# Kernel optimization log

Hardware: AMD Instinct MI355X
Metric: run time of the kernel (lower is better)

Reference implementation:

```python
import jax, jax.numpy as jnp
import numpy as np

B, N, DIN, DOUT, S, ITERS = 32, 2048, 512, 512, 2, 3
HID = max(DOUT, 128)  # mlp hidden = max(dim_out, hidden_dim)
EPS = 1e-8
LN_EPS = 1e-5  # torch LayerNorm default
SCALE = DOUT ** -0.5


def layernorm(x, g, b):
    m = jnp.mean(x, axis=-1, keepdims=True)
    v = jnp.mean(jnp.square(x - m), axis=-1, keepdims=True)
    return (x - m) * jax.lax.rsqrt(v + LN_EPS) * g + b


def setup_inputs() -> dict:
    key = jax.random.key(0)
    ks = jax.random.split(key, 16)
    w = lambda k, shp: jax.random.normal(k, shp, dtype=jnp.float32) * 0.02
    return {
        "inputs": jax.random.normal(ks[0], (B, N, DIN), dtype=jnp.float32),
        "shared_init_slots": jax.random.normal(ks[1], (B, S, DOUT), dtype=jnp.float32),
        "Wq": w(ks[2], (DOUT, DOUT)), "bq": jnp.zeros((DOUT,), jnp.float32),
        "Wk": w(ks[3], (DIN, DOUT)), "bk": jnp.zeros((DOUT,), jnp.float32),
        "Wv": w(ks[4], (DIN, DOUT)), "bv": jnp.zeros((DOUT,), jnp.float32),
        "ln_in_g": jnp.ones((DIN,), jnp.float32), "ln_in_b": jnp.zeros((DIN,), jnp.float32),
        "ln_s_g": jnp.ones((DOUT,), jnp.float32), "ln_s_b": jnp.zeros((DOUT,), jnp.float32),
        "ln_f_g": jnp.ones((DOUT,), jnp.float32), "ln_f_b": jnp.zeros((DOUT,), jnp.float32),
        "gru_wih": w(ks[5], (3 * DOUT, DOUT)), "gru_whh": w(ks[6], (3 * DOUT, DOUT)),
        "gru_bih": jnp.zeros((3 * DOUT,), jnp.float32), "gru_bhh": jnp.zeros((3 * DOUT,), jnp.float32),
        "W1": w(ks[7], (DOUT, HID)), "b1": jnp.zeros((HID,), jnp.float32),
        "W2": w(ks[8], (HID, DOUT)), "b2": jnp.zeros((DOUT,), jnp.float32),
    }


def reference(inputs, shared_init_slots, Wq, bq, Wk, bk, Wv, bv,
              ln_in_g, ln_in_b, ln_s_g, ln_s_b, ln_f_g, ln_f_b,
              gru_wih, gru_whh, gru_bih, gru_bhh, W1, b1, W2, b2):
    x = layernorm(inputs, ln_in_g, ln_in_b)          # [B,N,DIN]
    k = x @ Wk + bk                                   # [B,N,DOUT]
    v = x @ Wv + bv                                   # [B,N,DOUT]
    slots = shared_init_slots                         # [B,S,DOUT]
    for _ in range(ITERS):
        slots_prev = slots
        s = layernorm(slots, ln_s_g, ln_s_b)
        q = s @ Wq + bq                               # [B,S,DOUT]
        dots = jnp.einsum('bid,bjd->bij', q, k) * SCALE   # [B,S,N]
        attn_pre = jax.nn.softmax(dots, axis=1)       # softmax over SLOT dim (custom)
        attn = attn_pre / (jnp.sum(attn_pre, axis=-1, keepdims=True) + EPS)
        updates = jnp.einsum('bjd,bij->bid', v, attn)  # [B,S,DOUT]
        # GRUCell: h' = (1-z)*n + z*h, gate order r,z,n (torch convention)
        u = updates.reshape(-1, DOUT)
        h = slots_prev.reshape(-1, DOUT)
        gx = u @ gru_wih.T + gru_bih                  # [B*S, 3*DOUT]
        gh = h @ gru_whh.T + gru_bhh
        xr, xz, xn = jnp.split(gx, 3, axis=-1)
        hr, hz, hn = jnp.split(gh, 3, axis=-1)
        r = jax.nn.sigmoid(xr + hr)
        z = jax.nn.sigmoid(xz + hz)
        n_gate = jnp.tanh(xn + r * hn)
        h_new = (1.0 - z) * n_gate + z * h
        # residual MLP
        hln = layernorm(h_new, ln_f_g, ln_f_b)
        h_new = h_new + (jax.nn.relu(hln @ W1 + b1) @ W2 + b2)
        slots = h_new.reshape(B, S, DOUT)
    return slots, q, k, attn
```

## Files before the change

kernel.cpp:

```cpp
#include <hip/hip_runtime.h>
#include <stdint.h>

typedef __bf16 bf16_t;
typedef bf16_t bf16x8 __attribute__((ext_vector_type(8)));
typedef float f32x4 __attribute__((ext_vector_type(4)));

typedef unsigned int u32;
typedef __attribute__((address_space(1))) const u32 gu32;
typedef __attribute__((address_space(3))) u32 lu32;

#define LN_EPS 1e-5f
#define EPS_ 1e-8f
#define SCALE_ 0.04419417382415922f

__device__ __forceinline__ float wave_red_sum(float v) {
#pragma unroll
  for (int off = 32; off > 0; off >>= 1) v += __shfl_xor(v, off, 64);
  return v;
}

__global__ __launch_bounds__(256) void transpose_prep(
    const float* __restrict__ Wk, const float* __restrict__ Wv,
    const float* __restrict__ wih, const float* __restrict__ whh,
    bf16_t* __restrict__ BT, float* __restrict__ wihT, float* __restrict__ whhT)
{
  int z = blockIdx.z;
  if (z < 2 && blockIdx.y >= 16) return;
  const float* src = (z == 0) ? Wk : (z == 1) ? Wv : (z == 2) ? wih : whh;
  __shared__ float tile[32][33];
  int tx = threadIdx.x & 31, ty = threadIdx.x >> 5;
  int row0 = blockIdx.y * 32, col0 = blockIdx.x * 32;
#pragma unroll
  for (int i = 0; i < 4; ++i)
    tile[ty + 8 * i][tx] = src[(size_t)(row0 + ty + 8 * i) * 512 + col0 + tx];
  __syncthreads();
  if (z < 2) {
#pragma unroll
    for (int i = 0; i < 4; ++i)
      BT[(size_t)(z * 512 + col0 + ty + 8 * i) * 512 + row0 + tx] =
          (bf16_t)tile[tx][ty + 8 * i];
  } else {
    float* dst = (z == 2) ? wihT : whhT;
#pragma unroll
    for (int i = 0; i < 4; ++i)
      dst[(size_t)(col0 + ty + 8 * i) * 1536 + row0 + tx] = tile[tx][ty + 8 * i];
  }
}

__global__ __launch_bounds__(256) void small_prep(
    const float* __restrict__ bk, const float* __restrict__ bv,
    const float* __restrict__ slots_init,
    float* __restrict__ biasc, float* __restrict__ slots)
{
  int idx = blockIdx.x * 256 + threadIdx.x;
  if (idx < 1024) {
    biasc[idx] = (idx < 512) ? bk[idx] : bv[idx - 512];
  } else {
    int i = idx - 1024;
    slots[i] = slots_init[i];
  }
}

__global__ __launch_bounds__(256) void ln_apply(
    const float* __restrict__ in, const float* __restrict__ lng,
    const float* __restrict__ lnb, bf16_t* __restrict__ xbf)
{
  int w = threadIdx.x >> 6, lane = threadIdx.x & 63;
  size_t row = (size_t)blockIdx.x * 4 + w;
  const float4* rp = (const float4*)(in + row * 512);
  float4 a = rp[lane * 2], c = rp[lane * 2 + 1];
  float s1 = a.x + a.y + a.z + a.w + c.x + c.y + c.z + c.w;
  float s2 = a.x * a.x + a.y * a.y + a.z * a.z + a.w * a.w +
             c.x * c.x + c.y * c.y + c.z * c.z + c.w * c.w;
  s1 = wave_red_sum(s1);
  s2 = wave_red_sum(s2);
  float mean = s1 * (1.f / 512.f);
  float var = s2 * (1.f / 512.f) - mean * mean;
  float rs = rsqrtf(var + LN_EPS);
  float4 g0 = *(const float4*)&lng[lane * 8];
  float4 g1 = *(const float4*)&lng[lane * 8 + 4];
  float4 b0 = *(const float4*)&lnb[lane * 8];
  float4 b1 = *(const float4*)&lnb[lane * 8 + 4];
  bf16x8 o;
  o[0] = (bf16_t)((a.x - mean) * rs * g0.x + b0.x);
  o[1] = (bf16_t)((a.y - mean) * rs * g0.y + b0.y);
  o[2] = (bf16_t)((a.z - mean) * rs * g0.z + b0.z);
  o[3] = (bf16_t)((a.w - mean) * rs * g0.w + b0.w);
  o[4] = (bf16_t)((c.x - mean) * rs * g1.x + b1.x);
  o[5] = (bf16_t)((c.y - mean) * rs * g1.y + b1.y);
  o[6] = (bf16_t)((c.z - mean) * rs * g1.z + b1.z);
  o[7] = (bf16_t)((c.w - mean) * rs * g1.w + b1.w);
  *(bf16x8*)&xbf[row * 512 + lane * 8] = o;
}

__global__ __launch_bounds__(256) void gemm_kv(
    const bf16_t* __restrict__ xbf, const bf16_t* __restrict__ BT,
    const float* __restrict__ biasc,
    float* __restrict__ out_k, bf16_t* __restrict__ vbf, bf16_t* kbf)
{
  __shared__ __align__(16) char smem[32768];
  bf16_t* As = (bf16_t*)smem;
  bf16_t* Bs = (bf16_t*)(smem + 16384);
  float (*Cs)[132] = (float(*)[132])smem;

  const int tid = threadIdx.x, lane = tid & 63, w = tid >> 6;
  const int quad = lane >> 4, l16 = lane & 15;
  const int l = blockIdx.x;
  const int x = l & 7, t = l >> 3;
  const int n0 = (t & 7) * 128;
  const int m0 = ((t >> 3) * 8 + x) * 128;
  const int mb = (w & 1) * 64, nb = (w >> 1) * 64;
  const int swz = l16 & 7;

  const bf16_t* a_base = xbf + (size_t)m0 * 512;
  const bf16_t* b_base = BT + (size_t)n0 * 512;

  f32x4 acc[4][4] = {};

  for (int kk = 0; kk < 512; kk += 64) {
#pragma unroll
    for (int r = 0; r < 4; ++r) {
      int tt = tid + r * 256;
      int rr = tt >> 3, pg = tt & 7;
      int lg = pg ^ (rr & 7);
      __builtin_amdgcn_global_load_lds((gu32*)(a_base + (size_t)rr * 512 + kk + lg * 8),
                                       (lu32*)&As[tt * 8], 16, 0, 0);
      __builtin_amdgcn_global_load_lds((gu32*)(b_base + (size_t)rr * 512 + kk + lg * 8),
                                       (lu32*)&Bs[tt * 8], 16, 0, 0);
    }
    __syncthreads();
#pragma unroll
    for (int ks = 0; ks < 2; ++ks) {
      bf16x8 af[4], bfr[4];
#pragma unroll
      for (int mt = 0; mt < 4; ++mt)
        af[mt] = *(const bf16x8*)&As[(mb + mt * 16 + l16) * 64 + (((quad + 4 * ks) ^ swz) * 8)];
#pragma unroll
      for (int nt = 0; nt < 4; ++nt)
        bfr[nt] = *(const bf16x8*)&Bs[(nb + nt * 16 + l16) * 64 + (((quad + 4 * ks) ^ swz) * 8)];
#pragma unroll
      for (int mt = 0; mt < 4; ++mt)
#pragma unroll
        for (int nt = 0; nt < 4; ++nt)
          acc[mt][nt] = __builtin_amdgcn_mfma_f32_16x16x32_bf16(af[mt], bfr[nt], acc[mt][nt], 0, 0, 0);
    }
    __syncthreads();
  }

  const int is_k = (n0 < 512);
  const int col4 = (tid * 4) & 127;
  const int row8 = tid >> 4;
  const int col8 = (tid * 8) & 127;
  for (int ci = 0; ci < 8; ++ci) {
    if ((ci < 4) == (mb == 0)) {
      int mt = ci & 3;
#pragma unroll
      for (int nt = 0; nt < 4; ++nt)
#pragma unroll
        for (int r = 0; r < 4; ++r)
          Cs[quad * 4 + r][nb + nt * 16 + l16] = acc[mt][nt][r];
    }
    __syncthreads();
    int rowbase = m0 + ci * 16;
    if (is_k) {
      f32x4 bias4 = *(const f32x4*)&biasc[n0 + col4];
#pragma unroll
      for (int p = 0; p < 2; ++p) {
        int f = p * 1024 + tid * 4;
        int row = f >> 7;
        f32x4 v = *(const f32x4*)&Cs[row][col4] + bias4;
        *(f32x4*)&out_k[(size_t)(rowbase + row) * 512 + n0 + col4] = v;
      }
      if (kbf) {
        f32x4 ba = *(const f32x4*)&biasc[n0 + col8];
        f32x4 bb = *(const f32x4*)&biasc[n0 + col8 + 4];
        f32x4 v0 = *(const f32x4*)&Cs[row8][col8] + ba;
        f32x4 v1 = *(const f32x4*)&Cs[row8][col8 + 4] + bb;
        bf16x8 o;
#pragma unroll
        for (int j = 0; j < 4; ++j) { o[j] = (bf16_t)v0[j]; o[4 + j] = (bf16_t)v1[j]; }
        *(bf16x8*)&kbf[(size_t)(rowbase + row8) * 512 + n0 + col8] = o;
      }
    } else {
      f32x4 ba = *(const f32x4*)&biasc[n0 + col8];
      f32x4 bb = *(const f32x4*)&biasc[n0 + col8 + 4];
      f32x4 v0 = *(const f32x4*)&Cs[row8][col8] + ba;
      f32x4 v1 = *(const f32x4*)&Cs[row8][col8 + 4] + bb;
      bf16x8 o;
#pragma unroll
      for (int j = 0; j < 4; ++j) { o[j] = (bf16_t)v0[j]; o[4 + j] = (bf16_t)v1[j]; }
      *(bf16x8*)&vbf[(size_t)(rowbase + row8) * 512 + (n0 - 512) + col8] = o;
    }
    __syncthreads();
  }
}

__global__ __launch_bounds__(256) void ln_q_kernel(
    const float* __restrict__ slots,
    const float* __restrict__ lnsg, const float* __restrict__ lnsb,
    const float* __restrict__ Wq, const float* __restrict__ bq,
    float* __restrict__ q_out)
{
  __shared__ float s[2][512];
  __shared__ float part[4][2][64];
  __shared__ float red1[4], red2[4];
  int tid = threadIdx.x, w = tid >> 6, lane = tid & 63;
  int b = blockIdx.x >> 3, cg = blockIdx.x & 7;

  int r = tid >> 7;
  int off = (tid * 4) & 511;
  float4 v = *(const float4*)&slots[b * 1024 + tid * 4];
  float s1 = v.x + v.y + v.z + v.w;
  float s2 = v.x * v.x + v.y * v.y + v.z * v.z + v.w * v.w;
  s1 = wave_red_sum(s1);
  s2 = wave_red_sum(s2);
  if (lane == 0) { red1[w] = s1; red2[w] = s2; }
  __syncthreads();
  float mean = (red1[r * 2] + red1[r * 2 + 1]) * (1.f / 512.f);
  float var = (red2[r * 2] + red2[r * 2 + 1]) * (1.f / 512.f) - mean * mean;
  float rstd = rsqrtf(var + LN_EPS);
  float4 g4 = *(const float4*)&lnsg[off];
  float4 b4 = *(const float4*)&lnsb[off];
  s[r][off + 0] = (v.x - mean) * rstd * g4.x + b4.x;
  s[r][off + 1] = (v.y - mean) * rstd * g4.y + b4.y;
  s[r][off + 2] = (v.z - mean) * rstd * g4.z + b4.z;
  s[r][off + 3] = (v.w - mean) * rstd * g4.w + b4.w;
  __syncthreads();

  int c = cg * 64 + lane;
  float a0 = 0.f, a1 = 0.f;
  for (int d = w * 128; d < w * 128 + 128; ++d) {
    float wv = Wq[d * 512 + c];
    a0 += s[0][d] * wv;
    a1 += s[1][d] * wv;
  }
  part[w][0][lane] = a0;
  part[w][1][lane] = a1;
  __syncthreads();
  if (tid < 128) {
    int rr = tid >> 6, ll = tid & 63;
    float sum = part[0][rr][ll] + part[1][rr][ll] + part[2][rr][ll] + part[3][rr][ll]
              + bq[cg * 64 + ll];
    q_out[(b * 2 + rr) * 512 + cg * 64 + ll] = sum;
  }
}

__global__ __launch_bounds__(256) void attend_fused(
    const float* __restrict__ kf, const bf16_t* __restrict__ vbf,
    const float* __restrict__ qf,
    float* __restrict__ upd_part, float* __restrict__ rs_part,
    float* __restrict__ attn_pre)
{
  __shared__ float qs[2][528];
  __shared__ float p_s[2][64];
  int tid = threadIdx.x, w = tid >> 6, lane = tid & 63;
  int b = blockIdx.x >> 5, chunk = blockIdx.x & 31;
  int j0 = chunk * 64;

  {
    int slot = tid >> 7, pos = (tid & 127) * 4;
    int dq = pos >> 7, dd = pos & 127;
    *(f32x4*)&qs[slot][dq * 132 + dd] = *(const f32x4*)&qf[b * 1024 + slot * 512 + pos];
  }
  __syncthreads();

  int jj = lane & 15;
  int dq = lane >> 4;
  const float* kp = kf + (size_t)(b * 2048 + j0 + w * 16 + jj) * 512 + dq * 128;
  const float* qb0 = &qs[0][dq * 132];
  const float* qb1 = &qs[1][dq * 132];
  float dot0 = 0.f, dot1 = 0.f;
#pragma unroll
  for (int h = 0; h < 4; ++h) {
    f32x4 kr[8];
#pragma unroll
    for (int i = 0; i < 8; ++i) kr[i] = *(const f32x4*)(kp + h * 32 + i * 4);
#pragma unroll
    for (int i = 0; i < 8; ++i) {
      f32x4 qa = *(const f32x4*)(qb0 + h * 32 + i * 4);
      f32x4 qc = *(const f32x4*)(qb1 + h * 32 + i * 4);
#pragma unroll
      for (int t = 0; t < 4; ++t) {
        dot0 += kr[i][t] * qa[t];
        dot1 += kr[i][t] * qc[t];
      }
    }
  }
  dot0 += __shfl_xor(dot0, 16, 64);
  dot0 += __shfl_xor(dot0, 32, 64);
  dot1 += __shfl_xor(dot1, 16, 64);
  dot1 += __shfl_xor(dot1, 32, 64);
  float d0f = dot0 * SCALE_, d1f = dot1 * SCALE_;
  float mx = fmaxf(d0f, d1f);
  float e0 = __expf(d0f - mx), e1 = __expf(d1f - mx);
  float inv = 1.f / (e0 + e1);
  float p0 = e0 * inv, p1 = e1 * inv;
  if (lane < 16) {
    int jj2 = w * 16 + lane;
    p_s[0][jj2] = p0;
    p_s[1][jj2] = p1;
    attn_pre[(b * 2 + 0) * 2048 + j0 + jj2] = p0;
    attn_pre[(b * 2 + 1) * 2048 + j0 + jj2] = p1;
  }
  __syncthreads();

  if (w == 0) {
    float a = p_s[0][lane];
    float c = p_s[1][lane];
    a = wave_red_sum(a);
    c = wave_red_sum(c);
    if (lane == 0) {
      rs_part[(b * 2 + 0) * 32 + chunk] = a;
      rs_part[(b * 2 + 1) * 32 + chunk] = c;
    }
  }

  float u0[8] = {}, u1[8] = {};
  const bf16_t* vp = vbf + (size_t)(b * 2048 + j0 + w * 16) * 512 + lane * 8;
  for (int t = 0; t < 16; ++t) {
    float p0b = p_s[0][w * 16 + t];
    float p1b = p_s[1][w * 16 + t];
    bf16x8 vv = *(const bf16x8*)(vp + (size_t)t * 512);
#pragma unroll
    for (int tt = 0; tt < 8; ++tt) {
      float vfl = (float)vv[tt];
      u0[tt] += p0b * vfl;
      u1[tt] += p1b * vfl;
    }
  }
  float* up0 = upd_part + ((size_t)(chunk * 4 + w) * 64 + b * 2 + 0) * 512 + lane * 8;
  f32x4 w0a = {u0[0], u0[1], u0[2], u0[3]}, w0b = {u0[4], u0[5], u0[6], u0[7]};
  f32x4 w1a = {u1[0], u1[1], u1[2], u1[3]}, w1b = {u1[4], u1[5], u1[6], u1[7]};
  *(f32x4*)(up0) = w0a;
  *(f32x4*)(up0 + 4) = w0b;
  *(f32x4*)(up0 + 512) = w1a;
  *(f32x4*)(up0 + 516) = w1b;
}

__global__ __launch_bounds__(256) void attend_bf16(
    const bf16_t* __restrict__ kbf, const bf16_t* __restrict__ vbf,
    const float* __restrict__ qf,
    float* __restrict__ upd_part, float* __restrict__ rs_part,
    float* __restrict__ attn_pre)
{
  __shared__ float qs[2][528];
  __shared__ float p_s[2][64];
  int tid = threadIdx.x, w = tid >> 6, lane = tid & 63;
  int b = blockIdx.x >> 5, chunk = blockIdx.x & 31;
  int j0 = chunk * 64;

  {
    int slot = tid >> 7, pos = (tid & 127) * 4;
    int dq = pos >> 7, dd = pos & 127;
    *(f32x4*)&qs[slot][dq * 132 + dd] = *(const f32x4*)&qf[b * 1024 + slot * 512 + pos];
  }
  __syncthreads();

  int jj = lane & 15;
  int dq = lane >> 4;
  const bf16_t* kp = kbf + (size_t)(b * 2048 + j0 + w * 16 + jj) * 512 + dq * 128;
  const float* qb0 = &qs[0][dq * 132];
  const float* qb1 = &qs[1][dq * 132];
  float dot0 = 0.f, dot1 = 0.f;
#pragma unroll
  for (int h = 0; h < 2; ++h) {
    bf16x8 kr[8];
#pragma unroll
    for (int i = 0; i < 8; ++i) kr[i] = *(const bf16x8*)(kp + h * 64 + i * 8);
#pragma unroll
    for (int i = 0; i < 8; ++i) {
      f32x4 qa0 = *(const f32x4*)(qb0 + h * 64 + i * 8);
      f32x4 qa1 = *(const f32x4*)(qb0 + h * 64 + i * 8 + 4);
      f32x4 qc0 = *(const f32x4*)(qb1 + h * 64 + i * 8);
      f32x4 qc1 = *(const f32x4*)(qb1 + h * 64 + i * 8 + 4);
#pragma unroll
      for (int t = 0; t < 4; ++t) {
        float klo = (float)kr[i][t], khi = (float)kr[i][t + 4];
        dot0 += klo * qa0[t] + khi * qa1[t];
        dot1 += klo * qc0[t] + khi * qc1[t];
      }
    }
  }
  dot0 += __shfl_xor(dot0, 16, 64);
  dot0 += __shfl_xor(dot0, 32, 64);
  dot1 += __shfl_xor(dot1, 16, 64);
  dot1 += __shfl_xor(dot1, 32, 64);
  float d0f = dot0 * SCALE_, d1f = dot1 * SCALE_;
  float mx = fmaxf(d0f, d1f);
  float e0 = __expf(d0f - mx), e1 = __expf(d1f - mx);
  float inv = 1.f / (e0 + e1);
  float p0 = e0 * inv, p1 = e1 * inv;
  if (lane < 16) {
    int jj2 = w * 16 + lane;
    p_s[0][jj2] = p0;
    p_s[1][jj2] = p1;
    attn_pre[(b * 2 + 0) * 2048 + j0 + jj2] = p0;
    attn_pre[(b * 2 + 1) * 2048 + j0 + jj2] = p1;
  }
  __syncthreads();

  if (w == 0) {
    float a = p_s[0][lane];
    float c = p_s[1][lane];
    a = wave_red_sum(a);
    c = wave_red_sum(c);
    if (lane == 0) {
      rs_part[(b * 2 + 0) * 32 + chunk] = a;
      rs_part[(b * 2 + 1) * 32 + chunk] = c;
    }
  }

  float u0[8] = {}, u1[8] = {};
  const bf16_t* vp = vbf + (size_t)(b * 2048 + j0 + w * 16) * 512 + lane * 8;
  for (int t = 0; t < 16; ++t) {
    float p0b = p_s[0][w * 16 + t];
    float p1b = p_s[1][w * 16 + t];
    bf16x8 vv = *(const bf16x8*)(vp + (size_t)t * 512);
#pragma unroll
    for (int tt = 0; tt < 8; ++tt) {
      float vfl = (float)vv[tt];
      u0[tt] += p0b * vfl;
      u1[tt] += p1b * vfl;
    }
  }
  float* up0 = upd_part + ((size_t)(chunk * 4 + w) * 64 + b * 2 + 0) * 512 + lane * 8;
  f32x4 w0a = {u0[0], u0[1], u0[2], u0[3]}, w0b = {u0[4], u0[5], u0[6], u0[7]};
  f32x4 w1a = {u1[0], u1[1], u1[2], u1[3]}, w1b = {u1[4], u1[5], u1[6], u1[7]};
  *(f32x4*)(up0) = w0a;
  *(f32x4*)(up0 + 4) = w0b;
  *(f32x4*)(up0 + 512) = w1a;
  *(f32x4*)(up0 + 516) = w1b;
}

__global__ __launch_bounds__(512) void reduce_upd(
    const float* __restrict__ upd_part, const float* __restrict__ rs_part,
    float* __restrict__ upd, float* __restrict__ rowsum)
{
  int r = blockIdx.x, tid = threadIdx.x;
  const float* p = upd_part + (size_t)r * 512 + tid;
  float acc = 0.f;
#pragma unroll 8
  for (int i = 0; i < 128; ++i) acc += p[(size_t)i * 32768];
  upd[r * 512 + tid] = acc;
  if (tid < 64) {
    float v = (tid < 32) ? rs_part[r * 32 + tid] : 0.f;
    v = wave_red_sum(v);
    if (tid == 0) rowsum[r] = v;
  }
}

__global__ __launch_bounds__(256) void gates_kernel(
    const float* __restrict__ slots, const float* __restrict__ upd,
    const float* __restrict__ rowsum,
    const float* __restrict__ wihT, const float* __restrict__ whhT,
    const float* __restrict__ bih, const float* __restrict__ bhh,
    float* __restrict__ gx, float* __restrict__ gh)
{
  __shared__ float in_s[2][512];
  __shared__ float part[4][2][256];
  int tid = threadIdx.x, w = tid >> 6, lane = tid & 63;
  int rg = blockIdx.x / 12, cc = blockIdx.x % 12;
  int is_gh = (cc >= 6);
  int ccl = is_gh ? cc - 6 : cc;
  {
    int rr = tid >> 7, pos = (tid & 127) * 4;
    int row = rg * 2 + rr;
    const float* src = (is_gh ? slots : upd) + row * 512;
    f32x4 v = *(const f32x4*)&src[pos];
    if (!is_gh) v *= 1.f / (rowsum[row] + EPS_);
    *(f32x4*)&in_s[rr][pos] = v;
  }
  __syncthreads();
  int c0 = ccl * 256 + lane * 4;
  const float* __restrict__ W = is_gh ? whhT : wihT;
  f32x4 acc0 = {0.f, 0.f, 0.f, 0.f}, acc1 = acc0;
  for (int d = w * 128; d < w * 128 + 128; ++d) {
    f32x4 w4 = *(const f32x4*)&W[d * 1536 + c0];
    acc0 += in_s[0][d] * w4;
    acc1 += in_s[1][d] * w4;
  }
  *(f32x4*)&part[w][0][lane * 4] = acc0;
  *(f32x4*)&part[w][1][lane * 4] = acc1;
  __syncthreads();
  if (tid < 128) {
    int r = tid >> 6, ll = tid & 63;
    int cf = ccl * 256 + ll * 4;
    f32x4 s = *(const f32x4*)&part[0][r][ll * 4];
    s += *(const f32x4*)&part[1][r][ll * 4];
    s += *(const f32x4*)&part[2][r][ll * 4];
    s += *(const f32x4*)&part[3][r][ll * 4];
    s += *(const f32x4*)&(is_gh ? bhh : bih)[cf];
    *(f32x4*)&(is_gh ? gh : gx)[(rg * 2 + r) * 1536 + cf] = s;
  }
}

__global__ __launch_bounds__(512) void gru_ln_kernel(
    const float* __restrict__ gx, const float* __restrict__ gh,
    const float* __restrict__ slots,
    const float* __restrict__ lnf_g, const float* __restrict__ lnf_b,
    float* __restrict__ hnew, float* __restrict__ hln)
{
  __shared__ float red1[8], red2[8];
  int tid = threadIdx.x, row = blockIdx.x;
  float gxr = gx[row * 1536 + tid], gxz = gx[row * 1536 + 512 + tid], gxn = gx[row * 1536 + 1024 + tid];
  float ghr = gh[row * 1536 + tid], ghz = gh[row * 1536 + 512 + tid], ghn = gh[row * 1536 + 1024 + tid];
  float h = slots[row * 512 + tid];
  float r_ = 1.f / (1.f + __expf(-(gxr + ghr)));
  float z_ = 1.f / (1.f + __expf(-(gxz + ghz)));
  float n_ = tanhf(gxn + r_ * ghn);
  float hn = (1.f - z_) * n_ + z_ * h;
  hnew[row * 512 + tid] = hn;
  float s1 = wave_red_sum(hn), s2 = wave_red_sum(hn * hn);
  int w = tid >> 6, lane = tid & 63;
  if (lane == 0) { red1[w] = s1; red2[w] = s2; }
  __syncthreads();
  s1 = 0.f; s2 = 0.f;
#pragma unroll
  for (int i = 0; i < 8; ++i) { s1 += red1[i]; s2 += red2[i]; }
  float mean = s1 * (1.f / 512.f);
  float var = s2 * (1.f / 512.f) - mean * mean;
  float rstd = rsqrtf(var + LN_EPS);
  hln[row * 512 + tid] = (hn - mean) * rstd * lnf_g[tid] + lnf_b[tid];
}

__global__ __launch_bounds__(256) void mlp1_kernel(
    const float* __restrict__ hln, const float* __restrict__ W1,
    const float* __restrict__ b1, float* __restrict__ act)
{
  __shared__ float in_s[2][512];
  __shared__ float part[4][2][64];
  int tid = threadIdx.x, w = tid >> 6, lane = tid & 63;
  int rg = blockIdx.x >> 3, cc = blockIdx.x & 7;
  {
    int rr = tid >> 7, pos = (tid & 127) * 4;
    *(f32x4*)&in_s[rr][pos] = *(const f32x4*)&hln[(rg * 2 + rr) * 512 + pos];
  }
  __syncthreads();
  int c = cc * 64 + lane;
  float a0 = 0.f, a1 = 0.f;
  for (int d = w * 128; d < w * 128 + 128; ++d) {
    float wv = W1[d * 512 + c];
    a0 += in_s[0][d] * wv;
    a1 += in_s[1][d] * wv;
  }
  part[w][0][lane] = a0;
  part[w][1][lane] = a1;
  __syncthreads();
  if (tid < 128) {
    int r = tid >> 6, ll = tid & 63;
    float s = part[0][r][ll] + part[1][r][ll] + part[2][r][ll] + part[3][r][ll]
            + b1[cc * 64 + ll];
    act[(rg * 2 + r) * 512 + cc * 64 + ll] = fmaxf(s, 0.f);
  }
}

__global__ __launch_bounds__(256) void mlp2_kernel(
    const float* __restrict__ act, const float* __restrict__ W2,
    const float* __restrict__ b2, const float* __restrict__ hnew,
    float* __restrict__ slots)
{
  __shared__ float in_s[2][512];
  __shared__ float part[4][2][64];
  int tid = threadIdx.x, w = tid >> 6, lane = tid & 63;
  int rg = blockIdx.x >> 3, cc = blockIdx.x & 7;
  {
    int rr = tid >> 7, pos = (tid & 127) * 4;
    *(f32x4*)&in_s[rr][pos] = *(const f32x4*)&act[(rg * 2 + rr) * 512 + pos];
  }
  __syncthreads();
  int c = cc * 64 + lane;
  float a0 = 0.f, a1 = 0.f;
  for (int d = w * 128; d < w * 128 + 128; ++d) {
    float wv = W2[d * 512 + c];
    a0 += in_s[0][d] * wv;
    a1 += in_s[1][d] * wv;
  }
  part[w][0][lane] = a0;
  part[w][1][lane] = a1;
  __syncthreads();
  if (tid < 128) {
    int r = tid >> 6, ll = tid & 63;
    int row = rg * 2 + r, c2 = cc * 64 + ll;
    float s = part[0][r][ll] + part[1][r][ll] + part[2][r][ll] + part[3][r][ll] + b2[c2];
    slots[row * 512 + c2] = hnew[row * 512 + c2] + s;
  }
}

__global__ __launch_bounds__(256) void norm_attn(
    const float* __restrict__ rowsum, float* __restrict__ attn)
{
  int idx = blockIdx.x * 256 + threadIdx.x;
  int row = idx >> 11;
  attn[idx] = attn[idx] / (rowsum[row] + EPS_);
}

extern "C" void kernel_launch(void* const* d_in, const int* in_sizes, int n_in,
                              void* d_out, int out_size, void* d_ws, size_t ws_size,
                              hipStream_t stream)
{
  const float* inputs     = (const float*)d_in[0];
  const float* slots_init = (const float*)d_in[1];
  const float* Wq   = (const float*)d_in[2];
  const float* bq   = (const float*)d_in[3];
  const float* Wk   = (const float*)d_in[4];
  const float* bk   = (const float*)d_in[5];
  const float* Wv   = (const float*)d_in[6];
  const float* bv   = (const float*)d_in[7];
  const float* ln_in_g = (const float*)d_in[8];
  const float* ln_in_b = (const float*)d_in[9];
  const float* ln_s_g  = (const float*)d_in[10];
  const float* ln_s_b  = (const float*)d_in[11];
  const float* ln_f_g  = (const float*)d_in[12];
  const float* ln_f_b  = (const float*)d_in[13];
  const float* wih  = (const float*)d_in[14];
  const float* whh  = (const float*)d_in[15];
  const float* bih  = (const float*)d_in[16];
  const float* bhh  = (const float*)d_in[17];
  const float* W1   = (const float*)d_in[18];
  const float* b1   = (const float*)d_in[19];
  const float* W2   = (const float*)d_in[20];
  const float* b2   = (const float*)d_in[21];

  float* out   = (float*)d_out;
  float* slots = out;
  float* q_out = out + 32768;
  float* k_out = out + 65536;
  float* attnp = out + 33619968;

  char* ws = (char*)d_ws;
  bf16_t* xbf   = (bf16_t*)(ws);
  float*  upd_part = (float*)(ws);
  float*  rs_part  = (float*)(ws + 16777216);
  bf16_t* vbf   = (bf16_t*)(ws + 67108864);
  bf16_t* BT    = (bf16_t*)(ws + 134217728);
  float*  gx    = (float*)(ws + 134217728);
  float*  gh    = (float*)(ws + 134610944);
  float*  hnew  = (float*)(ws + 135004160);
  float*  hln   = (float*)(ws + 135135232);
  float*  wihT  = (float*)(ws + 135266304);
  float*  whhT  = (float*)(ws + 138412032);
  float*  biasc = (float*)(ws + 141557760);
  float*  act   = (float*)(ws + 141561856);
  float*  upd   = (float*)(ws + 142086144);
  float*  rowsum= (float*)(ws + 142217216);

  const size_t kbf_off = 142217472ull;
  const bool big_ws = ws_size >= kbf_off + 67108864ull;
  bf16_t* kbf = big_ws ? (bf16_t*)(ws + kbf_off) : (bf16_t*)nullptr;

  transpose_prep<<<dim3(16, 48, 4), 256, 0, stream>>>(Wk, Wv, wih, whh, BT, wihT, whhT);
  small_prep<<<132, 256, 0, stream>>>(bk, bv, slots_init, biasc, slots);
  ln_apply<<<16384, 256, 0, stream>>>(inputs, ln_in_g, ln_in_b, xbf);
  gemm_kv<<<4096, 256, 0, stream>>>(xbf, BT, biasc, k_out, vbf, kbf);
  for (int it = 0; it < 3; ++it) {
    ln_q_kernel<<<256, 256, 0, stream>>>(slots, ln_s_g, ln_s_b, Wq, bq, q_out);
    if (big_ws)
      attend_bf16<<<1024, 256, 0, stream>>>(kbf, vbf, q_out, upd_part, rs_part, attnp);
    else
      attend_fused<<<1024, 256, 0, stream>>>(k_out, vbf, q_out, upd_part, rs_part, attnp);
    reduce_upd<<<64, 512, 0, stream>>>(upd_part, rs_part, upd, rowsum);
    gates_kernel<<<384, 256, 0, stream>>>(slots, upd, rowsum, wihT, whhT, bih, bhh, gx, gh);
    gru_ln_kernel<<<64, 512, 0, stream>>>(gx, gh, slots, ln_f_g, ln_f_b, hnew, hln);
    mlp1_kernel<<<256, 256, 0, stream>>>(hln, W1, b1, act);
    mlp2_kernel<<<256, 256, 0, stream>>>(act, W2, b2, hnew, slots);
  }
  norm_attn<<<512, 256, 0, stream>>>(rowsum, attnp);
}
```

Baseline: 635.6 us.

## Double-buffer KV GEMM k-tiles and write epilogue directly from registers

The K/V projection GEMM now uses two 32-wide k-tile LDS buffers, issuing the async global-to-LDS load of the next tile before computing the current one, with one barrier per step instead of two. The LDS XOR swizzle is adjusted to the narrower 32-element rows. The epilogue no longer stages the accumulator through LDS with per-chunk barriers. It writes scalar fp32 and bf16 outputs straight from the MFMA registers, which gives up wide vectorized stores and may weaken coalescing.

```diff
diff --git a/kernel.cpp b/kernel.cpp
--- a/kernel.cpp
+++ b/kernel.cpp
@@ -99,99 +99,107 @@
     float* __restrict__ out_k, bf16_t* __restrict__ vbf, bf16_t* kbf)
 {
   __shared__ __align__(16) char smem[32768];
-  bf16_t* As = (bf16_t*)smem;
-  bf16_t* Bs = (bf16_t*)(smem + 16384);
-  float (*Cs)[132] = (float(*)[132])smem;
 
   const int tid = threadIdx.x, lane = tid & 63, w = tid >> 6;
   const int quad = lane >> 4, l16 = lane & 15;
   const int l = blockIdx.x;
-  const int x = l & 7, t = l >> 3;
-  const int n0 = (t & 7) * 128;
-  const int m0 = ((t >> 3) * 8 + x) * 128;
+  const int x = l & 7, t0 = l >> 3;
+  const int n0 = (t0 & 7) * 128;
+  const int m0 = ((t0 >> 3) * 8 + x) * 128;
   const int mb = (w & 1) * 64, nb = (w >> 1) * 64;
-  const int swz = l16 & 7;
+  const int swz = (l16 >> 1) & 3;
 
   const bf16_t* a_base = xbf + (size_t)m0 * 512;
   const bf16_t* b_base = BT + (size_t)n0 * 512;
 
   f32x4 acc[4][4] = {};
 
-  for (int kk = 0; kk < 512; kk += 64) {
-#pragma unroll
-    for (int r = 0; r < 4; ++r) {
+  auto stage = [&](int buf, int kk) {
+    bf16_t* As = (bf16_t*)(smem + buf * 16384);
+    bf16_t* Bs = (bf16_t*)(smem + buf * 16384 + 8192);
+#pragma unroll
+    for (int r = 0; r < 2; ++r) {
       int tt = tid + r * 256;
-      int rr = tt >> 3, pg = tt & 7;
-      int lg = pg ^ (rr & 7);
+      int rr = tt >> 2, pg = tt & 3;
+      int lg = pg ^ ((rr >> 1) & 3);
       __builtin_amdgcn_global_load_lds((gu32*)(a_base + (size_t)rr * 512 + kk + lg * 8),
                                        (lu32*)&As[tt * 8], 16, 0, 0);
       __builtin_amdgcn_global_load_lds((gu32*)(b_base + (size_t)rr * 512 + kk + lg * 8),
                                        (lu32*)&Bs[tt * 8], 16, 0, 0);
     }
-    __syncthreads();
-#pragma unroll
-    for (int ks = 0; ks < 2; ++ks) {
-      bf16x8 af[4], bfr[4];
-#pragma unroll
-      for (int mt = 0; mt < 4; ++mt)
-        af[mt] = *(const bf16x8*)&As[(mb + mt * 16 + l16) * 64 + (((quad + 4 * ks) ^ swz) * 8)];
+  };
+
+  auto compute = [&](int buf) {
+    const bf16_t* As = (const bf16_t*)(smem + buf * 16384);
+    const bf16_t* Bs = (const bf16_t*)(smem + buf * 16384 + 8192);
+    bf16x8 af[4], bfr[4];
+#pragma unroll
+    for (int mt = 0; mt < 4; ++mt)
+      af[mt] = *(const bf16x8*)&As[(mb + mt * 16 + l16) * 32 + ((quad ^ swz) * 8)];
+#pragma unroll
+    for (int nt = 0; nt < 4; ++nt)
+      bfr[nt] = *(const bf16x8*)&Bs[(nb + nt * 16 + l16) * 32 + ((quad ^ swz) * 8)];
+#pragma unroll
+    for (int mt = 0; mt < 4; ++mt)
 #pragma unroll
       for (int nt = 0; nt < 4; ++nt)
-        bfr[nt] = *(const bf16x8*)&Bs[(nb + nt * 16 + l16) * 64 + (((quad + 4 * ks) ^ swz) * 8)];
-#pragma unroll
-      for (int mt = 0; mt < 4; ++mt)
-#pragma unroll
-        for (int nt = 0; nt < 4; ++nt)
-          acc[mt][nt] = __builtin_amdgcn_mfma_f32_16x16x32_bf16(af[mt], bfr[nt], acc[mt][nt], 0, 0, 0);
-    }
-    __syncthreads();
+        acc[mt][nt] = __builtin_amdgcn_mfma_f32_16x16x32_bf16(af[mt], bfr[nt], acc[mt][nt], 0, 0, 0);
+  };
+
+  stage(0, 0);
+  __syncthreads();
+#pragma unroll
+  for (int t = 0; t < 16; ++t) {
+    if (t < 15) stage((t + 1) & 1, (t + 1) * 32);
+    compute(t & 1);
+    if (t < 15) __syncthreads();
   }
 
   const int is_k = (n0 < 512);
-  const int col4 = (tid * 4) & 127;
-  const int row8 = tid >> 4;
-  const int col8 = (tid * 8) & 127;
-  for (int ci = 0; ci < 8; ++ci) {
-    if ((ci < 4) == (mb == 0)) {
-      int mt = ci & 3;
-#pragma unroll
-      for (int nt = 0; nt < 4; ++nt)
+  const int rbase = m0 + mb + quad * 4;
+  if (is_k) {
+#pragma unroll
+    for (int nt = 0; nt < 4; ++nt) {
+      int col = n0 + nb + nt * 16 + l16;
+      float bias = biasc[col];
+#pragma unroll
+      for (int mt = 0; mt < 4; ++mt) {
+        int row = rbase + mt * 16;
+#pragma unroll
+        for (int r = 0; r < 4; ++r) {
+          float v = acc[mt][nt][r] + bias;
+          out_k[(size_t)(row + r) * 512 + col] = v;
+        }
+      }
+    }
+    if (kbf) {
+#pragma unroll
+      for (int nt = 0; nt < 4; ++nt) {
+        int col = n0 + nb + nt * 16 + l16;
+        float bias = biasc[col];
+#pragma unroll
+        for (int mt = 0; mt < 4; ++mt) {
+          int row = rbase + mt * 16;
+#pragma unroll
+          for (int r = 0; r < 4; ++r)
+            kbf[(size_t)(row + r) * 512 + col] = (bf16_t)(acc[mt][nt][r] + bias);
+        }
+      }
+    }
+  } else {
+#pragma unroll
+    for (int nt = 0; nt < 4; ++nt) {
+      int colg = n0 + nb + nt * 16 + l16;
+      float bias = biasc[colg];
+      int col = colg - 512;
+#pragma unroll
+      for (int mt = 0; mt < 4; ++mt) {
+        int row = rbase + mt * 16;
 #pragma unroll
         for (int r = 0; r < 4; ++r)
-          Cs[quad * 4 + r][nb + nt * 16 + l16] = acc[mt][nt][r];
-    }
-    __syncthreads();
-    int rowbase = m0 + ci * 16;
-    if (is_k) {
-      f32x4 bias4 = *(const f32x4*)&biasc[n0 + col4];
-#pragma unroll
-      for (int p = 0; p < 2; ++p) {
-        int f = p * 1024 + tid * 4;
-        int row = f >> 7;
-        f32x4 v = *(const f32x4*)&Cs[row][col4] + bias4;
-        *(f32x4*)&out_k[(size_t)(rowbase + row) * 512 + n0 + col4] = v;
+          vbf[(size_t)(row + r) * 512 + col] = (bf16_t)(acc[mt][nt][r] + bias);
       }
-      if (kbf) {
-        f32x4 ba = *(const f32x4*)&biasc[n0 + col8];
-        f32x4 bb = *(const f32x4*)&biasc[n0 + col8 + 4];
-        f32x4 v0 = *(const f32x4*)&Cs[row8][col8] + ba;
-        f32x4 v1 = *(const f32x4*)&Cs[row8][col8 + 4] + bb;
-        bf16x8 o;
-#pragma unroll
-        for (int j = 0; j < 4; ++j) { o[j] = (bf16_t)v0[j]; o[4 + j] = (bf16_t)v1[j]; }
-        *(bf16x8*)&kbf[(size_t)(rowbase + row8) * 512 + n0 + col8] = o;
-      }
-    } else {
-      f32x4 ba = *(const f32x4*)&biasc[n0 + col8];
-      f32x4 bb = *(const f32x4*)&biasc[n0 + col8 + 4];
-      f32x4 v0 = *(const f32x4*)&Cs[row8][col8] + ba;
-      f32x4 v1 = *(const f32x4*)&Cs[row8][col8 + 4] + bb;
-      bf16x8 o;
-#pragma unroll
-      for (int j = 0; j < 4; ++j) { o[j] = (bf16_t)v0[j]; o[4 + j] = (bf16_t)v1[j]; }
-      *(bf16x8*)&vbf[(size_t)(rowbase + row8) * 512 + (n0 - 512) + col8] = o;
-    }
-    __syncthreads();
+    }
   }
 }
 
```

Result: faster. 617.6 us (-2.8%).
